# Performance work log

Measured on AMD Instinct MI355X. Metric: run time of the kernel, lower is better.

## Reference

```python
import jax, jax.numpy as jnp
import numpy as np
import math

V, T, E, N = 32000, 128, 64, 1024
SIGMA_MIN, SIGMA_MAX, C = 0.1, 10.0, 2.0


def setup_inputs() -> dict:
    key = jax.random.key(0)
    k1, k2, k3, k4, k5 = jax.random.split(key, 5)
    return {
        "x": jax.random.normal(k1, (T, N), dtype=jnp.float32),
        "mu": jax.random.normal(k2, (V, E), dtype=jnp.float32),
        "log_sigma": jax.random.normal(k3, (V, E), dtype=jnp.float32),
        "mu_c": jax.random.normal(k4, (T, E), dtype=jnp.float32),
        "log_sigma_c": jax.random.normal(k5, (T, E), dtype=jnp.float32),
        "t": 0,
    }


def reference(x, mu, log_sigma, mu_c, log_sigma_c, t):
    # parameter clamping done in-place in the torch forward
    bound = math.sqrt(C)
    mu = jnp.clip(mu, -bound, bound)
    mu_c = jnp.clip(mu_c, -bound, bound)
    log_sigma = jnp.clip(log_sigma, math.log(SIGMA_MIN), math.log(SIGMA_MAX))
    log_sigma_c = jnp.clip(log_sigma_c, math.log(SIGMA_MIN), math.log(SIGMA_MAX))

    sigma = jnp.exp(log_sigma)        # [V, E]
    sigma_c = jnp.exp(log_sigma_c)    # [T, E]

    # pairwise Gaussian expected-likelihood energy, vectorized over topics
    s = sigma[:, None, :] + sigma_c[None, :, :]            # [V, T, E]
    det_fac = jnp.sum(jnp.log(s), axis=-1)                 # [V, T]
    diff = mu[:, None, :] - mu_c[None, :, :]               # [V, T, E]
    diff_mu = jnp.sum(diff * diff / s, axis=-1)            # [V, T]
    emb_dim = mu.shape[-1]
    log_el = -0.5 * (det_fac + diff_mu + emb_dim * math.log(2.0 * math.pi))

    # per-topic softmax over the vocab axis
    w = jax.nn.softmax(log_el, axis=0)                     # [V, T]

    return w @ x.reshape(-1, x.shape[-1])                  # [V, N]
```

## Files before the change

kernel.cpp:

```cpp
#include <hip/hip_runtime.h>
#include <math.h>

#define VV 32000
#define TT 128
#define EE 64
#define NN 1024
#define NPART 500

static constexpr float BOUND    = 1.41421356237309515f;
static constexpr float LOG_SMIN = -2.30258509299404568f;
static constexpr float LOG_SMAX =  2.30258509299404568f;
static constexpr float LN2      =  0.69314718055994531f;
static constexpr float LOG2E    =  1.44269504088896340f;
static constexpr float E_LOG2PI =  64.0f * 1.83787706640934548f;

typedef __attribute__((ext_vector_type(2)))  float f32x2;
typedef __attribute__((ext_vector_type(8)))  short short8;
typedef __attribute__((ext_vector_type(16))) float float16;

static __device__ inline unsigned short f2bf(float f) {
    union { float f; unsigned u; } v; v.f = f;
    unsigned r = v.u + 0x7FFFu + ((v.u >> 16) & 1u);
    return (unsigned short)(r >> 16);
}

static __device__ inline unsigned pack_bf16(float a, float b) {
    unsigned r;
    asm("v_cvt_pk_bf16_f32 %0, %1, %2" : "=v"(r) : "v"(a), "v"(b));
    return r;
}

__global__ __launch_bounds__(256) void prep_xpose(const float* __restrict__ mu_c,
                                                  const float* __restrict__ log_sigma_c,
                                                  const float* __restrict__ x,
                                                  float* __restrict__ sc,
                                                  float* __restrict__ mc,
                                                  unsigned short* __restrict__ xT) {
    const int tid = threadIdx.x;
    if (blockIdx.x < 32) {
        int i = blockIdx.x * 256 + tid;
        if (i < TT * EE) {
            float ls = log_sigma_c[i];
            ls = fminf(fmaxf(ls, LOG_SMIN), LOG_SMAX);
            sc[i] = __expf(ls);
            float m = mu_c[i];
            mc[i] = fminf(fmaxf(m, -BOUND), BOUND);
        }
    } else {
        const int b = blockIdx.x - 32;
        const int n = b * 32 + (tid & 31);
        const int th = tid >> 5;
        const float* __restrict__ xp = x + n;
#pragma unroll
        for (int i = 0; i < 16; i += 2) {
            int t = th * 16 + i;
            float x0 = xp[(size_t)t * NN];
            float x1 = xp[(size_t)(t + 1) * NN];
            *(unsigned*)&xT[n * TT + t] = (unsigned)f2bf(x0) | ((unsigned)f2bf(x1) << 16);
        }
    }
}

__global__ __launch_bounds__(256) void logits_kernel(const float* __restrict__ mu,
                                                     const float* __restrict__ log_sigma,
                                                     const float* __restrict__ sc,
                                                     const float* __restrict__ mc,
                                                     float* __restrict__ logitsVT,
                                                     float* __restrict__ pm,
                                                     float* __restrict__ pl) {
    __shared__ float part[16][4][64];
    __shared__ float lvt[64][33];
    const int tid  = threadIdx.x;
    const int lane = tid & 63;
    const int wv   = tid >> 6;
    const int v0   = blockIdx.x * 64;
    const int t0   = blockIdx.y * 32;
    const int e0u  = __builtin_amdgcn_readfirstlane(wv) * 16;

    f32x2 sv[8], mv[8];
    {
        const float* __restrict__ lsp = log_sigma + (size_t)(v0 + lane) * EE + e0u;
        const float* __restrict__ mup = mu        + (size_t)(v0 + lane) * EE + e0u;
#pragma unroll
        for (int j = 0; j < 8; j++) {
            float a = lsp[2 * j], b = lsp[2 * j + 1];
            a = fminf(fmaxf(a, LOG_SMIN), LOG_SMAX);
            b = fminf(fmaxf(b, LOG_SMIN), LOG_SMAX);
            sv[j] = f32x2{__expf(a), __expf(b)};
            float c = mup[2 * j], d = mup[2 * j + 1];
            mv[j] = f32x2{fminf(fmaxf(c, -BOUND), BOUND), fminf(fmaxf(d, -BOUND), BOUND)};
        }
    }

    f32x2 cs[2][8], cm[2][8];
    {
        const f32x2* __restrict__ sp = (const f32x2*)(sc + t0 * EE + e0u);
        const f32x2* __restrict__ mp = (const f32x2*)(mc + t0 * EE + e0u);
#pragma unroll
        for (int j = 0; j < 8; j++) { cs[0][j] = sp[j]; cm[0][j] = mp[j]; }
    }

    for (int tb = 0; tb < 2; tb++) {
#pragma unroll
        for (int i = 0; i < 16; i++) {
            const int ti  = tb * 16 + i;
            const int cur = ti & 1;
            if (ti < 31) {
                const int tn = t0 + ti + 1;
                const f32x2* __restrict__ sp = (const f32x2*)(sc + tn * EE + e0u);
                const f32x2* __restrict__ mp = (const f32x2*)(mc + tn * EE + e0u);
#pragma unroll
                for (int j = 0; j < 8; j++) { cs[cur ^ 1][j] = sp[j]; cm[cur ^ 1][j] = mp[j]; }
            }
            f32x2 q = {0.f, 0.f};
            f32x2 p = {1.f, 1.f};
#pragma unroll
            for (int j = 0; j < 8; j++) {
                f32x2 s = sv[j] + cs[cur][j];
                p *= s;
                f32x2 d = mv[j] - cm[cur][j];
                f32x2 r;
                r.x = __builtin_amdgcn_rcpf(s.x);
                r.y = __builtin_amdgcn_rcpf(s.y);
                q += d * d * r;
            }
            part[i][wv][lane] = __log2f(p.x * p.y) * LN2 + q.x + q.y;
        }
        __syncthreads();
#pragma unroll
        for (int k = 0; k < 4; k++) {
            const int i = wv * 4 + k;
            const int t = t0 + tb * 16 + i;
            float sum = part[i][0][lane] + part[i][1][lane] + part[i][2][lane] + part[i][3][lane];
            float logit = -0.5f * (sum + E_LOG2PI);
            lvt[lane][tb * 16 + i] = logit;

            float m = logit;
#pragma unroll
            for (int off = 1; off < 64; off <<= 1) m = fmaxf(m, __shfl_xor(m, off));
            float sx = __expf(logit - m);
#pragma unroll
            for (int off = 1; off < 64; off <<= 1) sx += __shfl_xor(sx, off);
            if (lane == 0) {
                pm[t * NPART + blockIdx.x] = m;
                pl[t * NPART + blockIdx.x] = sx;
            }
        }
        __syncthreads();
    }

    {
        const int v  = tid >> 2;
        const int c0 = (tid & 3) * 8;
        float4 d0, d1;
        d0.x = lvt[v][c0 + 0]; d0.y = lvt[v][c0 + 1];
        d0.z = lvt[v][c0 + 2]; d0.w = lvt[v][c0 + 3];
        d1.x = lvt[v][c0 + 4]; d1.y = lvt[v][c0 + 5];
        d1.z = lvt[v][c0 + 6]; d1.w = lvt[v][c0 + 7];
        float* dst = logitsVT + (size_t)(v0 + v) * TT + t0 + c0;
        *(float4*)dst       = d0;
        *(float4*)(dst + 4) = d1;
    }
}

__global__ __launch_bounds__(256) void merge_stats(const float* __restrict__ pm,
                                                   const float* __restrict__ pl,
                                                   float* __restrict__ stats) {
    const int tid = threadIdx.x;
    const int t = blockIdx.x;
    __shared__ float red[8];
    float m = -3.4e38f;
    for (int j = tid; j < NPART; j += 256) m = fmaxf(m, pm[t * NPART + j]);
#pragma unroll
    for (int off = 1; off < 64; off <<= 1) m = fmaxf(m, __shfl_xor(m, off));
    if ((tid & 63) == 0) red[tid >> 6] = m;
    __syncthreads();
    m = fmaxf(fmaxf(red[0], red[1]), fmaxf(red[2], red[3]));

    float l = 0.0f;
    for (int j = tid; j < NPART; j += 256)
        l += pl[t * NPART + j] * __expf(pm[t * NPART + j] - m);
#pragma unroll
    for (int off = 1; off < 64; off <<= 1) l += __shfl_xor(l, off);
    if ((tid & 63) == 0) red[4 + (tid >> 6)] = l;
    __syncthreads();
    if (tid == 0) {
        float tot = red[4] + red[5] + red[6] + red[7];
        stats[t] = -(__log2f(tot) + m * LOG2E);
    }
}

__global__ __launch_bounds__(256) void wx_mfma(const float* __restrict__ logitsVT,
                                               const float* __restrict__ stats,
                                               const unsigned short* __restrict__ xT,
                                               float* __restrict__ out) {
    const int g  = blockIdx.x;
    const int x8 = g & 7;
    const int k  = g >> 3;
    const int vt = x8 * 64 + (k >> 3);
    const int nc = k & 7;
    if (vt >= VV / 64) return;

    const int tid = threadIdx.x;
    const int n0 = nc * 128;
    const int v0 = vt * 64;
    const int lane = tid & 63;
    const int wv   = tid >> 6;
    const int vh   = (wv & 1) * 32;
    const int nh   = (wv >> 1) * 64;
    const int r32  = lane & 31;
    const int koff = (lane >> 5) * 8;

    const float* __restrict__ lp = logitsVT + (size_t)(v0 + vh + r32) * TT + koff;
    const float* __restrict__ cp = stats + koff;
    const unsigned short* __restrict__ bp0 = xT + (size_t)(n0 + nh + r32) * TT + koff;
    const unsigned short* __restrict__ bp1 = bp0 + 32 * TT;

    float16 acc0 = {0,0,0,0,0,0,0,0,0,0,0,0,0,0,0,0};
    float16 acc1 = {0,0,0,0,0,0,0,0,0,0,0,0,0,0,0,0};
#pragma unroll
    for (int kb = 0; kb < 8; kb++) {
        float4 l0 = *(const float4*)(lp + kb * 16);
        float4 l1 = *(const float4*)(lp + kb * 16 + 4);
        float c[8];
#pragma unroll
        for (int j = 0; j < 8; j++) c[j] = cp[kb * 16 + j];

        union { short8 v; unsigned u[4]; } a;
        a.u[0] = pack_bf16(exp2f(fmaf(l0.x, LOG2E, c[0])), exp2f(fmaf(l0.y, LOG2E, c[1])));
        a.u[1] = pack_bf16(exp2f(fmaf(l0.z, LOG2E, c[2])), exp2f(fmaf(l0.w, LOG2E, c[3])));
        a.u[2] = pack_bf16(exp2f(fmaf(l1.x, LOG2E, c[4])), exp2f(fmaf(l1.y, LOG2E, c[5])));
        a.u[3] = pack_bf16(exp2f(fmaf(l1.z, LOG2E, c[6])), exp2f(fmaf(l1.w, LOG2E, c[7])));

        short8 b0 = *(const short8*)(bp0 + kb * 16);
        short8 b1 = *(const short8*)(bp1 + kb * 16);
        acc0 = __builtin_amdgcn_mfma_f32_32x32x16_bf16(a.v, b0, acc0, 0, 0, 0);
        acc1 = __builtin_amdgcn_mfma_f32_32x32x16_bf16(a.v, b1, acc1, 0, 0, 0);
    }

    const int col = lane & 31;
    const int rbase = 4 * (lane >> 5);
#pragma unroll
    for (int r = 0; r < 16; r++) {
        int row = (r & 3) + 8 * (r >> 2) + rbase;
        float* dst = out + (size_t)(v0 + vh + row) * NN + n0 + nh + col;
        dst[0]  = acc0[r];
        dst[32] = acc1[r];
    }
}

extern "C" void kernel_launch(void* const* d_in, const int* in_sizes, int n_in,
                              void* d_out, int out_size, void* d_ws, size_t ws_size,
                              hipStream_t stream) {
    const float* x           = (const float*)d_in[0];
    const float* mu          = (const float*)d_in[1];
    const float* log_sigma   = (const float*)d_in[2];
    const float* mu_c        = (const float*)d_in[3];
    const float* log_sigma_c = (const float*)d_in[4];
    float* out = (float*)d_out;

    float* ws       = (float*)d_ws;
    float* logitsVT = ws;
    float* pm       = logitsVT + (size_t)TT * VV;
    float* pl       = pm + (size_t)TT * NPART;
    float* stats    = pl + (size_t)TT * NPART;
    float* sc       = stats + TT;
    float* mc       = sc + TT * EE;
    unsigned short* xT = (unsigned short*)(mc + TT * EE);

    prep_xpose<<<64, 256, 0, stream>>>(mu_c, log_sigma_c, x, sc, mc, xT);
    logits_kernel<<<dim3(VV / 64, 4), 256, 0, stream>>>(mu, log_sigma, sc, mc,
                                                        logitsVT, pm, pl);
    merge_stats<<<TT, 256, 0, stream>>>(pm, pl, stats);
    wx_mfma<<<4096, 256, 0, stream>>>(logitsVT, stats, xT, out);
}
```

Before: 254.3 us.

## Widen wx_mfma N tile to 256 and stage output through LDS for coalesced stores

Each block now covers 64 V rows by 256 N columns instead of 128, so the exp/bf16 conversion of the softmax weights (A operand) is computed once and reused across four MFMA tiles per wave. The grid is halved accordingly. Output is written through a shared-memory staging tile with float4 row-contiguous stores instead of strided scalar stores. The change costs more accumulator registers (64 floats per lane) and two barriers per half, which may reduce occupancy.

```diff
diff --git a/kernel.cpp b/kernel.cpp
--- a/kernel.cpp
+++ b/kernel.cpp
@@ -194,58 +194,81 @@
                                                const float* __restrict__ stats,
                                                const unsigned short* __restrict__ xT,
                                                float* __restrict__ out) {
+    __shared__ float lvt[32][256];
     const int g  = blockIdx.x;
-    const int x8 = g & 7;
-    const int k  = g >> 3;
-    const int vt = x8 * 64 + (k >> 3);
-    const int nc = k & 7;
+    const int id = (g & 7) * 256 + (g >> 3);
+    const int vt = id >> 2;
+    const int nc = id & 3;
     if (vt >= VV / 64) return;
 
     const int tid = threadIdx.x;
-    const int n0 = nc * 128;
+    const int n0 = nc * 256;
     const int v0 = vt * 64;
     const int lane = tid & 63;
     const int wv   = tid >> 6;
     const int vh   = (wv & 1) * 32;
-    const int nh   = (wv >> 1) * 64;
+    const int nh   = (wv >> 1) * 128;
     const int r32  = lane & 31;
     const int koff = (lane >> 5) * 8;
 
-    const float* __restrict__ lp = logitsVT + (size_t)(v0 + vh + r32) * TT + koff;
-    const float* __restrict__ cp = stats + koff;
-    const unsigned short* __restrict__ bp0 = xT + (size_t)(n0 + nh + r32) * TT + koff;
-    const unsigned short* __restrict__ bp1 = bp0 + 32 * TT;
-
-    float16 acc0 = {0,0,0,0,0,0,0,0,0,0,0,0,0,0,0,0};
-    float16 acc1 = {0,0,0,0,0,0,0,0,0,0,0,0,0,0,0,0};
+    short8 a[8];
+    {
+        const float* __restrict__ lp = logitsVT + (size_t)(v0 + vh + r32) * TT + koff;
+        const float* __restrict__ cp = stats + koff;
+#pragma unroll
+        for (int kb = 0; kb < 8; kb++) {
+            float4 l0 = *(const float4*)(lp + kb * 16);
+            float4 l1 = *(const float4*)(lp + kb * 16 + 4);
+            float c[8];
+#pragma unroll
+            for (int j = 0; j < 8; j++) c[j] = cp[kb * 16 + j];
+            union { short8 v; unsigned u[4]; } t;
+            t.u[0] = pack_bf16(exp2f(fmaf(l0.x, LOG2E, c[0])), exp2f(fmaf(l0.y, LOG2E, c[1])));
+            t.u[1] = pack_bf16(exp2f(fmaf(l0.z, LOG2E, c[2])), exp2f(fmaf(l0.w, LOG2E, c[3])));
+            t.u[2] = pack_bf16(exp2f(fmaf(l1.x, LOG2E, c[4])), exp2f(fmaf(l1.y, LOG2E, c[5])));
+            t.u[3] = pack_bf16(exp2f(fmaf(l1.z, LOG2E, c[6])), exp2f(fmaf(l1.w, LOG2E, c[7])));
+            a[kb] = t.v;
+        }
+    }
+
+    const unsigned short* __restrict__ bp = xT + (size_t)(n0 + nh + r32) * TT + koff;
+    float16 acc[4];
+#pragma unroll
+    for (int nt = 0; nt < 4; nt++) acc[nt] = (float16){0,0,0,0,0,0,0,0,0,0,0,0,0,0,0,0};
 #pragma unroll
     for (int kb = 0; kb < 8; kb++) {
-        float4 l0 = *(const float4*)(lp + kb * 16);
-        float4 l1 = *(const float4*)(lp + kb * 16 + 4);
-        float c[8];
-#pragma unroll
-        for (int j = 0; j < 8; j++) c[j] = cp[kb * 16 + j];
-
-        union { short8 v; unsigned u[4]; } a;
-        a.u[0] = pack_bf16(exp2f(fmaf(l0.x, LOG2E, c[0])), exp2f(fmaf(l0.y, LOG2E, c[1])));
-        a.u[1] = pack_bf16(exp2f(fmaf(l0.z, LOG2E, c[2])), exp2f(fmaf(l0.w, LOG2E, c[3])));
-        a.u[2] = pack_bf16(exp2f(fmaf(l1.x, LOG2E, c[4])), exp2f(fmaf(l1.y, LOG2E, c[5])));
-        a.u[3] = pack_bf16(exp2f(fmaf(l1.z, LOG2E, c[6])), exp2f(fmaf(l1.w, LOG2E, c[7])));
-
-        short8 b0 = *(const short8*)(bp0 + kb * 16);
-        short8 b1 = *(const short8*)(bp1 + kb * 16);
-        acc0 = __builtin_amdgcn_mfma_f32_32x32x16_bf16(a.v, b0, acc0, 0, 0, 0);
-        acc1 = __builtin_amdgcn_mfma_f32_32x32x16_bf16(a.v, b1, acc1, 0, 0, 0);
-    }
-
-    const int col = lane & 31;
+        short8 b0 = *(const short8*)(bp + (size_t)0 * 32 * TT + kb * 16);
+        short8 b1 = *(const short8*)(bp + (size_t)1 * 32 * TT + kb * 16);
+        short8 b2 = *(const short8*)(bp + (size_t)2 * 32 * TT + kb * 16);
+        short8 b3 = *(const short8*)(bp + (size_t)3 * 32 * TT + kb * 16);
+        acc[0] = __builtin_amdgcn_mfma_f32_32x32x16_bf16(a[kb], b0, acc[0], 0, 0, 0);
+        acc[1] = __builtin_amdgcn_mfma_f32_32x32x16_bf16(a[kb], b1, acc[1], 0, 0, 0);
+        acc[2] = __builtin_amdgcn_mfma_f32_32x32x16_bf16(a[kb], b2, acc[2], 0, 0, 0);
+        acc[3] = __builtin_amdgcn_mfma_f32_32x32x16_bf16(a[kb], b3, acc[3], 0, 0, 0);
+    }
+
+    const int col   = lane & 31;
     const int rbase = 4 * (lane >> 5);
 #pragma unroll
-    for (int r = 0; r < 16; r++) {
-        int row = (r & 3) + 8 * (r >> 2) + rbase;
-        float* dst = out + (size_t)(v0 + vh + row) * NN + n0 + nh + col;
-        dst[0]  = acc0[r];
-        dst[32] = acc1[r];
+    for (int half = 0; half < 2; half++) {
+        if ((wv & 1) == half) {
+#pragma unroll
+            for (int nt = 0; nt < 4; nt++) {
+#pragma unroll
+                for (int r = 0; r < 16; r++) {
+                    int row = (r & 3) + 8 * (r >> 2) + rbase;
+                    lvt[row][nh + nt * 32 + col] = acc[nt][r];
+                }
+            }
+        }
+        __syncthreads();
+#pragma unroll
+        for (int j = 0; j < 8; j++) {
+            int row = wv + j * 4;
+            float4 d = *(const float4*)&lvt[row][lane * 4];
+            *(float4*)(out + (size_t)(v0 + half * 32 + row) * NN + n0 + lane * 4) = d;
+        }
+        __syncthreads();
     }
 }
 
@@ -272,5 +295,5 @@
     logits_kernel<<<dim3(VV / 64, 4), 256, 0, stream>>>(mu, log_sigma, sc, mc,
                                                         logitsVT, pm, pl);
     merge_stats<<<TT, 256, 0, stream>>>(pm, pl, stats);
-    wx_mfma<<<4096, 256, 0, stream>>>(logitsVT, stats, xT, out);
-}
+    wx_mfma<<<2048, 256, 0, stream>>>(logitsVT, stats, xT, out);
+}
```

Measured after the change: 238.2 us. -6.4%, faster.
